# Kernel optimization log

Measured on AMD Instinct MI355X. Metric: run time of the kernel, lower is better.

The kernel has to match this reference:

```python
import jax, jax.numpy as jnp
import numpy as np

B, N, C, KV = 4, 4096, 1024, 1024
H = 4            # hardcoded 4-way split in the source
Ch, Kh = C // H, KV // H
EPS = 1e-5       # InstanceNorm2d default eps


def setup_inputs() -> dict:
    key = jax.random.key(0)
    ks = jax.random.split(key, 12)
    s = 0.02
    return {
        "emb1":     jax.random.normal(ks[0], (B, N, C),  jnp.float32),
        "emb_all":  jax.random.normal(ks[1], (B, N, KV), jnp.float32),
        "embd1":    jax.random.normal(ks[2], (B, N, C),  jnp.float32),
        "emb_alld": jax.random.normal(ks[3], (B, N, KV), jnp.float32),
        # per-head query weights (distinct per split), torch Linear layout [out,in]
        "Wq":   jax.random.normal(ks[4],  (H, Ch, Ch), jnp.float32) * s,
        "Wqd":  jax.random.normal(ks[5],  (H, Ch, Ch), jnp.float32) * s,
        # source reuses key[0]/value[0] for all splits -> single shared weight
        "Wk0":  jax.random.normal(ks[6],  (Kh, Kh), jnp.float32) * s,
        "Wv0":  jax.random.normal(ks[7],  (Kh, Kh), jnp.float32) * s,
        "Wkd0": jax.random.normal(ks[8],  (Kh, Kh), jnp.float32) * s,
        "Wvd0": jax.random.normal(ks[9],  (Kh, Kh), jnp.float32) * s,
        "Wout":  jax.random.normal(ks[10], (C, C), jnp.float32) * s,
        "Woutd": jax.random.normal(ks[11], (C, C), jnp.float32) * s,
    }


def _inorm(s):
    # InstanceNorm2d(affine=False): normalize over the (C/4, KV/4) plane per (b, head)
    m = s.mean(axis=(2, 3), keepdims=True)
    v = ((s - m) ** 2).mean(axis=(2, 3), keepdims=True)
    return (s - m) * jax.lax.rsqrt(v + EPS)


def reference(emb1, emb_all, embd1, emb_alld,
              Wq, Wqd, Wk0, Wv0, Wkd0, Wvd0, Wout, Woutd):
    scale = 1.0 / np.sqrt(KV).astype(np.float32)
    # split into 4 channel groups and project (Q: per-group weight; K/V: shared weight)
    Q  = jnp.einsum('bnhc,hoc->bhno', emb1.reshape(B, N, H, Ch),  Wq)    # [B,H,N,Ch]
    Qd = jnp.einsum('bnhc,hoc->bhno', embd1.reshape(B, N, H, Ch), Wqd)
    K  = jnp.einsum('bnhk,ok->bhno', emb_all.reshape(B, N, H, Kh),  Wk0)  # [B,H,N,Kh]
    V  = jnp.einsum('bnhk,ok->bhno', emb_all.reshape(B, N, H, Kh),  Wv0)
    Kd = jnp.einsum('bnhk,ok->bhno', emb_alld.reshape(B, N, H, Kh), Wkd0)
    Vd = jnp.einsum('bnhk,ok->bhno', emb_alld.reshape(B, N, H, Kh), Wvd0)
    # channel-attention scores: contract over tokens N -> [B,H,Ch,Kh]
    s1  = jnp.einsum('bhnc,bhnk->bhck', Q,  Kd) * scale
    sd1 = jnp.einsum('bhnc,bhnk->bhck', Qd, K)  * scale
    p1  = jax.nn.softmax(_inorm(s1),  axis=-1)
    pd1 = jax.nn.softmax(_inorm(sd1), axis=-1)
    # context: probs @ V^T -> [b,h,c,n]; permute(0,3,2,1)+view -> [B,N,C] (c-major, h-minor)
    ctx1  = jnp.einsum('bhck,bhnk->bnch', p1,  Vd).reshape(B, N, C)
    ctxd1 = jnp.einsum('bhck,bhnk->bnch', pd1, V ).reshape(B, N, C)
    O1  = ctx1  @ Wout.T
    Od1 = ctxd1 @ Woutd.T
    return (O1, Od1)
```

## Files before the change

### kernel.cpp

```cpp
#include <hip/hip_runtime.h>
#include <math.h>


#define PITCH 40

typedef __bf16 bf16x4 __attribute__((ext_vector_type(4)));
typedef __bf16 bf16x8 __attribute__((ext_vector_type(8)));
typedef float f32x4 __attribute__((ext_vector_type(4)));

__device__ inline void gl2lds16(const void* g, void* l) {
    __builtin_amdgcn_global_load_lds(
        (const __attribute__((address_space(1))) unsigned int*)g,
        (__attribute__((address_space(3))) unsigned int*)l, 16, 0, 0);
}

__global__ __launch_bounds__(256) void prep_x(const float* __restrict__ emb_all,
                                              const float* __restrict__ emb_alld,
                                              __bf16* __restrict__ Xb) {
    const float* src = blockIdx.y ? emb_alld : emb_all;
    __bf16* dst = Xb + (long long)blockIdx.y * 16777216;
    long long i4 = (long long)blockIdx.x * 256 + threadIdx.x;
    float4 v = *(const float4*)&src[i4 * 4];
    bf16x4 o = {(__bf16)v.x, (__bf16)v.y, (__bf16)v.z, (__bf16)v.w};
    *(bf16x4*)&dst[i4 * 4] = o;
}

__global__ __launch_bounds__(256) void prep_w(
    const float* __restrict__ Wq, const float* __restrict__ Wqd,
    const float* __restrict__ Wk0, const float* __restrict__ Wv0,
    const float* __restrict__ Wkd0, const float* __restrict__ Wvd0,
    const float* __restrict__ Wout, const float* __restrict__ Woutd,
    __bf16* __restrict__ Wq_bf, __bf16* __restrict__ Wk_bf,
    __bf16* __restrict__ WvT_bf, __bf16* __restrict__ WoutR_bf)
{
    int id = blockIdx.x * 256 + threadIdx.x;
    if (id < 524288) {
        Wq_bf[id] = (__bf16)(id < 262144 ? Wq[id] : Wqd[id - 262144]);
    } else if (id < 655360) {
        int j = id - 524288;
        Wk_bf[j] = (__bf16)(j < 65536 ? Wkd0[j] : Wk0[j - 65536]);
    } else if (id < 786432) {
        int j = id - 655360;
        int p = j >> 16, r = (j >> 8) & 255, c2 = j & 255;
        const float* s = p ? Wv0 : Wvd0;
        WvT_bf[j] = (__bf16)s[c2 * 256 + r];
    } else if (id < 2883584) {
        int j = id - 786432;
        int p = j >> 20; int rem = j & 1048575; int h = rem >> 18; int oc = rem & 262143;
        int o = oc >> 8, c = oc & 255;
        const float* s = p ? Woutd : Wout;
        WoutR_bf[j] = (__bf16)s[o * 1024 + c * 4 + h];
    }
}

__global__ __launch_bounds__(256) void gram_mfma(
    const float* __restrict__ emb1, const float* __restrict__ emb_all,
    const float* __restrict__ embd1, const float* __restrict__ emb_alld,
    float* __restrict__ Gpart)
{
    __shared__ __bf16 As[128 * PITCH];
    __shared__ __bf16 Bs[128 * PITCH];

    const int z = blockIdx.z;
    const int path = z >> 4, bh = z & 15;
    const int b = bh >> 2, h = bh & 3;
    const float* Xm = (path == 0 ? emb_alld : emb_all) + (long long)b * 4194304 + h * 256;
    const float* Xn = (path == 0 ? emb1     : embd1)   + (long long)b * 4194304 + h * 256;

    const int i0 = (blockIdx.x >> 1) * 128;
    const int j0 = (blockIdx.x & 1) * 128;
    const int kb0 = blockIdx.y * 1024;

    const int t = threadIdx.x;
    const int q  = t & 7;
    const int i4 = t >> 3;
    const int lane = t & 63;
    const int wave = t >> 6;
    const int wr = (wave >> 1) * 64, wc = (wave & 1) * 64;
    const int fm = lane & 15, fg = lane >> 4;

    f32x4 acc[4][4];
#pragma unroll
    for (int u = 0; u < 4; ++u)
#pragma unroll
        for (int v = 0; v < 4; ++v) acc[u][v] = (f32x4){0.f, 0.f, 0.f, 0.f};

    for (int kb = kb0; kb < kb0 + 1024; kb += 32) {
        float4 va[4], vb[4];
        const float* pa = Xm + (long long)(kb + q * 4) * 1024 + i0 + i4 * 4;
        const float* pb = Xn + (long long)(kb + q * 4) * 1024 + j0 + i4 * 4;
#pragma unroll
        for (int r = 0; r < 4; ++r) {
            va[r] = *(const float4*)(pa + (long long)r * 1024);
            vb[r] = *(const float4*)(pb + (long long)r * 1024);
        }
        __syncthreads();
#pragma unroll
        for (int c = 0; c < 4; ++c) {
            bf16x4 wa, wb;
#pragma unroll
            for (int r = 0; r < 4; ++r) {
                wa[r] = (__bf16)(((const float*)&va[r])[c]);
                wb[r] = (__bf16)(((const float*)&vb[r])[c]);
            }
            *(bf16x4*)&As[(i4 * 4 + c) * PITCH + q * 4] = wa;
            *(bf16x4*)&Bs[(i4 * 4 + c) * PITCH + q * 4] = wb;
        }
        __syncthreads();

        bf16x8 af[4], bfv[4];
#pragma unroll
        for (int mt = 0; mt < 4; ++mt)
            af[mt] = *(const bf16x8*)&As[(wr + mt * 16 + fm) * PITCH + fg * 8];
#pragma unroll
        for (int nt = 0; nt < 4; ++nt)
            bfv[nt] = *(const bf16x8*)&Bs[(wc + nt * 16 + fm) * PITCH + fg * 8];
#pragma unroll
        for (int mt = 0; mt < 4; ++mt)
#pragma unroll
            for (int nt = 0; nt < 4; ++nt)
                acc[mt][nt] = __builtin_amdgcn_mfma_f32_16x16x32_bf16(af[mt], bfv[nt], acc[mt][nt], 0, 0, 0);
    }

    float* Gp = Gpart + ((long long)blockIdx.y * 32 + z) * 65536;
    const int col = lane & 15, rq = (lane >> 4) * 4;
#pragma unroll
    for (int mt = 0; mt < 4; ++mt)
#pragma unroll
        for (int nt = 0; nt < 4; ++nt)
#pragma unroll
            for (int r = 0; r < 4; ++r)
                Gp[(i0 + wr + mt * 16 + rq + r) * 256 + (j0 + wc + nt * 16 + col)] = acc[mt][nt][r];
}

__global__ __launch_bounds__(256) void reduce_g(const float* __restrict__ Gpart, __bf16* __restrict__ GT) {
    long long idx4 = (long long)blockIdx.x * 256 + threadIdx.x;
    float4 a = *(const float4*)&Gpart[idx4 * 4];
    float4 b = *(const float4*)&Gpart[2097152 + idx4 * 4];
    float4 c = *(const float4*)&Gpart[4194304 + idx4 * 4];
    float4 d = *(const float4*)&Gpart[6291456 + idx4 * 4];
    bf16x4 o;
    o[0] = (__bf16)(a.x + b.x + c.x + d.x);
    o[1] = (__bf16)(a.y + b.y + c.y + d.y);
    o[2] = (__bf16)(a.z + b.z + c.z + d.z);
    o[3] = (__bf16)(a.w + b.w + c.w + d.w);
    *(bf16x4*)&GT[idx4 * 4] = o;
}

template <typename CT>
__global__ __launch_bounds__(256) void mfma_nt(
    const __bf16* __restrict__ A, const __bf16* __restrict__ B, CT* __restrict__ C,
    int mtiles, int K,
    long long a1, long long a2, long long a3,
    long long b1, long long b2, long long b3,
    long long c1, long long c2, long long c3,
    int cpitch, float alpha)
{
    __shared__ __bf16 As[64 * 32];
    __shared__ __bf16 Bs[64 * 32];
    const int z = blockIdx.y;
    const __bf16* Az = A + (long long)(z >> 4) * a1 + (long long)((z >> 2) & 3) * a2 + (long long)(z & 3) * a3;
    const __bf16* Bz = B + (long long)(z >> 4) * b1 + (long long)((z >> 2) & 3) * b2 + (long long)(z & 3) * b3;
    CT* Cz = C + (long long)(z >> 4) * c1 + (long long)((z >> 2) & 3) * c2 + (long long)(z & 3) * c3;

    const int tm = blockIdx.x % mtiles, tn = blockIdx.x / mtiles;
    const int t = threadIdx.x;
    const int lane = t & 63, wave = t >> 6;
    const int row = t >> 2, ch = t & 3;
    const int fm = lane & 15, fg = lane >> 4;

    const __bf16* ga = Az + (long long)(tm * 64 + row) * K + ch * 8;
    const __bf16* gb = Bz + (long long)(tn * 64 + row) * K + ch * 8;
    __bf16* la = &As[t * 8];
    __bf16* lb = &Bs[t * 8];

    f32x4 acc[4];
#pragma unroll
    for (int u = 0; u < 4; ++u) acc[u] = (f32x4){0.f, 0.f, 0.f, 0.f};

    for (int kb = 0; kb < K; kb += 32) {
        __syncthreads();
        gl2lds16(ga + kb, la);
        gl2lds16(gb + kb, lb);
        __syncthreads();
        bf16x8 bv = *(const bf16x8*)&Bs[(wave * 16 + fm) * 32 + fg * 8];
#pragma unroll
        for (int mt = 0; mt < 4; ++mt) {
            bf16x8 av = *(const bf16x8*)&As[(mt * 16 + fm) * 32 + fg * 8];
            acc[mt] = __builtin_amdgcn_mfma_f32_16x16x32_bf16(av, bv, acc[mt], 0, 0, 0);
        }
    }

    const int colc = tn * 64 + wave * 16 + fm;
    const int rq = fg * 4;
#pragma unroll
    for (int mt = 0; mt < 4; ++mt)
#pragma unroll
        for (int r = 0; r < 4; ++r) {
            int rowc = tm * 64 + mt * 16 + rq + r;
            Cz[(long long)rowc * cpitch + colc] = (CT)(acc[mt][r] * alpha);
        }
}


#define VMCNT8 asm volatile("s_waitcnt vmcnt(8)" ::: "memory")
#define VMCNT0 asm volatile("s_waitcnt vmcnt(0)" ::: "memory")
#define BARR   asm volatile("s_barrier" ::: "memory")

#define STAGE_A(h, kt, c) do { \
    _Pragma("unroll") \
    for (int o = 0; o < 2; ++o) { \
        int rl = (h) * 64 + o * 128 + stg_row; \
        gl2lds16(Xa + (long long)rl * 1024 + (kt) * 64 + stg_col, \
                 &lds[(c) * 32768 + rl * 64 + lin_col]); \
    } \
} while (0)

#define STAGE_B(h, kt, c) do { \
    _Pragma("unroll") \
    for (int o = 0; o < 2; ++o) { \
        int rl = o * 128 + (h) * 32 + (stg_row & 31) + ((stg_row & 32) << 1); \
        gl2lds16(Bb + (long long)rl * 1024 + (kt) * 64 + stg_col, \
                 &lds[(c) * 32768 + 16384 + rl * 64 + lin_col]); \
    } \
} while (0)

#define LOAD_A(hm, c) do { \
    _Pragma("unroll") \
    for (int mt = 0; mt < 4; ++mt) { \
        const __bf16* p = &lds[(c) * 32768 + (wr * 128 + (hm) * 64 + mt * 16 + fm) * 64]; \
        af[mt][0] = *(const bf16x8*)&p[(fg * 8) ^ rsw]; \
        af[mt][1] = *(const bf16x8*)&p[(32 + fg * 8) ^ rsw]; \
    } \
} while (0)

#define LOAD_B(hn, c) do { \
    _Pragma("unroll") \
    for (int nt = 0; nt < 2; ++nt) { \
        const __bf16* p = &lds[(c) * 32768 + 16384 + (wc * 64 + (hn) * 32 + nt * 16 + fm) * 64]; \
        bv[(hn) * 2 + nt][0] = *(const bf16x8*)&p[(fg * 8) ^ rsw]; \
        bv[(hn) * 2 + nt][1] = *(const bf16x8*)&p[(32 + fg * 8) ^ rsw]; \
    } \
} while (0)

#define MFMA_Q(hm, hn) do { \
    __builtin_amdgcn_s_setprio(1); \
    _Pragma("unroll") \
    for (int mt = 0; mt < 4; ++mt) \
        _Pragma("unroll") \
        for (int nt = 0; nt < 2; ++nt) { \
            acc[(hm) * 4 + mt][(hn) * 2 + nt] = __builtin_amdgcn_mfma_f32_16x16x32_bf16( \
                af[mt][0], bv[(hn) * 2 + nt][0], acc[(hm) * 4 + mt][(hn) * 2 + nt], 0, 0, 0); \
            acc[(hm) * 4 + mt][(hn) * 2 + nt] = __builtin_amdgcn_mfma_f32_16x16x32_bf16( \
                af[mt][1], bv[(hn) * 2 + nt][1], acc[(hm) * 4 + mt][(hn) * 2 + nt], 0, 0, 0); \
        } \
    __builtin_amdgcn_s_setprio(0); \
} while (0)

__global__ __launch_bounds__(512, 2) void obig8(
    const __bf16* __restrict__ Xall, const __bf16* __restrict__ Mb, float* __restrict__ out)
{
    __shared__ __bf16 lds[65536];

    const int id = blockIdx.x;
    const int wg = (id & 7) * 64 + (id >> 3);
    const int z = wg >> 6;
    const int tile = wg & 63;
    const int tm = tile & 15, tn = tile >> 4;
    const int path = z >> 2, b = z & 3;

    const __bf16* Xa = Xall + (path == 0 ? 16777216LL : 0LL)
                     + (long long)b * 4194304 + (long long)tm * 262144;
    const __bf16* Bb = Mb + (long long)path * 4194304 + (long long)b * 1048576
                     + (long long)tn * 262144;
    float* Ob = out + (long long)path * 16777216 + (long long)b * 4194304;

    const int t = threadIdx.x;
    const int lane = t & 63, wave = t >> 6;
    const int wr = wave >> 2, wc = wave & 3;
    const int fm = lane & 15, fg = lane >> 4;
    const int stg_row = t >> 3;
    const int lin_col = (t & 7) * 8;
    const int stg_col = ((t & 7) ^ (stg_row & 7)) * 8;
    const int rsw = (fm & 7) * 8;

    f32x4 acc[8][4];
#pragma unroll
    for (int u = 0; u < 8; ++u)
#pragma unroll
        for (int v = 0; v < 4; ++v) acc[u][v] = (f32x4){0.f, 0.f, 0.f, 0.f};

    bf16x8 af[4][2];
    bf16x8 bv[8][2];

    STAGE_A(0, 0, 0); STAGE_B(0, 0, 0); STAGE_B(1, 0, 0); STAGE_A(1, 0, 0);
    STAGE_A(0, 1, 1); STAGE_B(0, 1, 1); STAGE_B(1, 1, 1); STAGE_A(1, 1, 1);
    VMCNT8;
    BARR;

    for (int kt = 0; kt < 14; ++kt) {
        const int c = kt & 1;
        LOAD_A(0, c);
        LOAD_B(0, c);
        BARR;
        MFMA_Q(0, 0);
        BARR;
        LOAD_B(1, c);
        STAGE_A(0, kt + 2, c);
        BARR;
        MFMA_Q(0, 1);
        BARR;
        LOAD_A(1, c);
        STAGE_B(0, kt + 2, c);
        BARR;
        MFMA_Q(1, 1);
        BARR;
        STAGE_B(1, kt + 2, c);
        STAGE_A(1, kt + 2, c);
        VMCNT8;
        BARR;
        MFMA_Q(1, 0);
        BARR;
    }

    {
        LOAD_A(0, 0);
        LOAD_B(0, 0);
        BARR;
        MFMA_Q(0, 0);
        BARR;
        LOAD_B(1, 0);
        BARR;
        MFMA_Q(0, 1);
        BARR;
        LOAD_A(1, 0);
        BARR;
        MFMA_Q(1, 1);
        BARR;
        VMCNT0;
        BARR;
        MFMA_Q(1, 0);
        BARR;
    }

    {
        LOAD_A(0, 1);
        LOAD_B(0, 1);
        MFMA_Q(0, 0);
        LOAD_B(1, 1);
        MFMA_Q(0, 1);
        LOAD_A(1, 1);
        MFMA_Q(1, 1);
        MFMA_Q(1, 0);
    }

    const int rq = fg * 4;
    float* op = Ob + (long long)(tm * 256 + wr * 128 + rq) * 1024 + tn * 256 + wc * 64 + fm;
#pragma unroll
    for (int mi = 0; mi < 8; ++mi)
#pragma unroll
        for (int ni = 0; ni < 4; ++ni)
#pragma unroll
            for (int r = 0; r < 4; ++r)
                op[(long long)(mi * 16 + r) * 1024 + ni * 16] = acc[mi][ni][r];
}

__global__ __launch_bounds__(256) void stats_kernel(const float* __restrict__ S, float* __restrict__ st) {
    int pg = blockIdx.x;
    const float* s = S + (long long)pg * 65536;
    float sum = 0.f, sq = 0.f;
    for (int i = threadIdx.x; i < 65536; i += 256) {
        float v = s[i];
        sum += v;
        sq += v * v;
    }
#pragma unroll
    for (int off = 32; off; off >>= 1) {
        sum += __shfl_down(sum, off);
        sq  += __shfl_down(sq,  off);
    }
    __shared__ float r1[4], r2[4];
    int w = threadIdx.x >> 6;
    if ((threadIdx.x & 63) == 0) { r1[w] = sum; r2[w] = sq; }
    __syncthreads();
    if (threadIdx.x == 0) {
        float ts = r1[0] + r1[1] + r1[2] + r1[3];
        float tq = r2[0] + r2[1] + r2[2] + r2[3];
        float mean = ts * (1.0f / 65536.0f);
        float var = tq * (1.0f / 65536.0f) - mean * mean;
        st[pg * 2 + 0] = mean;
        st[pg * 2 + 1] = rsqrtf(var + 1e-5f);
    }
}

__global__ __launch_bounds__(256) void softmax_kernel(const float* __restrict__ S,
                                                      const float* __restrict__ st,
                                                      __bf16* __restrict__ p_bf) {
    int pg = blockIdx.y;
    int c = blockIdx.x;
    float mean = st[pg * 2 + 0], rstd = st[pg * 2 + 1];
    const float* row = S + (long long)pg * 65536 + c * 256;
    int t = threadIdx.x;
    float x = (row[t] - mean) * rstd;
    float m = x;
#pragma unroll
    for (int off = 32; off; off >>= 1) m = fmaxf(m, __shfl_down(m, off));
    __shared__ float r1[4], r2[4];
    int w = t >> 6;
    if ((t & 63) == 0) r1[w] = m;
    __syncthreads();
    m = fmaxf(fmaxf(r1[0], r1[1]), fmaxf(r1[2], r1[3]));
    float e = expf(x - m);
    float ssum = e;
#pragma unroll
    for (int off = 32; off; off >>= 1) ssum += __shfl_down(ssum, off);
    if ((t & 63) == 0) r2[w] = ssum;
    __syncthreads();
    ssum = r2[0] + r2[1] + r2[2] + r2[3];
    p_bf[(long long)pg * 65536 + c * 256 + t] = (__bf16)(e / ssum);
}

extern "C" void kernel_launch(void* const* d_in, const int* in_sizes, int n_in,
                              void* d_out, int out_size, void* d_ws, size_t ws_size,
                              hipStream_t stream) {
    const float* emb1     = (const float*)d_in[0];
    const float* emb_all  = (const float*)d_in[1];
    const float* embd1    = (const float*)d_in[2];
    const float* emb_alld = (const float*)d_in[3];
    const float* Wq    = (const float*)d_in[4];
    const float* Wqd   = (const float*)d_in[5];
    const float* Wk0   = (const float*)d_in[6];
    const float* Wv0   = (const float*)d_in[7];
    const float* Wkd0  = (const float*)d_in[8];
    const float* Wvd0  = (const float*)d_in[9];
    const float* Wout  = (const float*)d_in[10];
    const float* Woutd = (const float*)d_in[11];
    float* out = (float*)d_out;

    float* ws = (float*)d_ws;
    float*  Gpart   = ws;
    __bf16* Mb_bf   = (__bf16*)ws;
    __bf16* X_bf    = (__bf16*)(ws + 8388608);
    __bf16* GT_bf   = (__bf16*)(ws + 25165824);
    __bf16* T_bf    = (__bf16*)(ws + 26214400);
    float*  S       = ws + 27262976;
    __bf16* p_bf    = (__bf16*)(ws + 29360128);
    __bf16* PT_bf   = (__bf16*)(ws + 30408704);
    __bf16* Wq_bf   = (__bf16*)(ws + 31457280);
    __bf16* Wk_bf   = (__bf16*)(ws + 31719424);
    __bf16* WvT_bf  = (__bf16*)(ws + 31784960);
    __bf16* WoutR_bf= (__bf16*)(ws + 31850496);
    float*  st      = ws + 32899072;

    dim3 blk(256);

    prep_x<<<dim3(16384, 2), blk, 0, stream>>>(emb_all, emb_alld, X_bf);
    prep_w<<<11264, blk, 0, stream>>>(Wq, Wqd, Wk0, Wv0, Wkd0, Wvd0, Wout, Woutd,
                                      Wq_bf, Wk_bf, WvT_bf, WoutR_bf);

    gram_mfma<<<dim3(4, 4, 32), blk, 0, stream>>>(emb1, emb_all, embd1, emb_alld, Gpart);
    reduce_g<<<2048, blk, 0, stream>>>(Gpart, GT_bf);

    mfma_nt<__bf16><<<dim3(16, 32), blk, 0, stream>>>(
        Wq_bf, GT_bf, T_bf, 4, 256,
        262144, 0, 65536,  1048576, 262144, 65536,  1048576, 262144, 65536, 256, 1.0f);
    mfma_nt<float><<<dim3(16, 32), blk, 0, stream>>>(
        T_bf, Wk_bf, S, 4, 256,
        1048576, 262144, 65536,  65536, 0, 0,  1048576, 262144, 65536, 256, 0.03125f);

    stats_kernel<<<32, blk, 0, stream>>>(S, st);
    softmax_kernel<<<dim3(256, 32), blk, 0, stream>>>(S, st, p_bf);

    mfma_nt<__bf16><<<dim3(16, 32), blk, 0, stream>>>(
        WvT_bf, p_bf, PT_bf, 4, 256,
        65536, 0, 0,  1048576, 262144, 65536,  1048576, 262144, 65536, 256, 1.0f);
    mfma_nt<__bf16><<<dim3(64, 32), blk, 0, stream>>>(
        WoutR_bf, PT_bf, Mb_bf, 16, 256,
        1048576, 0, 262144,  1048576, 262144, 65536,  4194304, 1048576, 256, 1024, 1.0f);

    obig8<<<dim3(512), dim3(512), 0, stream>>>(X_bf, Mb_bf, out);
}
```

Measured before the change: 567.9 us.

## Double-buffer gram kernel loads and parallelize instance-norm stats and softmax

The gram kernel now keeps two register sets and two LDS buffers, so global loads for the next k-slice are issued while the current slice is converted and fed to MFMA, and one of the two barriers per step is dropped. The stats kernel is split across 8 chunks per plane with float4 loads, and the softmax kernel folds those partials together. Softmax now handles one row per wave with shuffle-xor reductions instead of a block-wide reduction over shared memory. This trades more registers and LDS in the gram kernel (it also declares a min-blocks hint of 2) for less load latency exposure and less serial work in the small kernels.

Result: faster. 507.5 us (-10.6%).

```diff
diff --git a/kernel.cpp b/kernel.cpp
--- a/kernel.cpp
+++ b/kernel.cpp
@@ -53,13 +53,13 @@
     }
 }
 
-__global__ __launch_bounds__(256) void gram_mfma(
+__global__ __launch_bounds__(256, 2) void gram_mfma(
     const float* __restrict__ emb1, const float* __restrict__ emb_all,
     const float* __restrict__ embd1, const float* __restrict__ emb_alld,
     float* __restrict__ Gpart)
 {
-    __shared__ __bf16 As[128 * PITCH];
-    __shared__ __bf16 Bs[128 * PITCH];
+    __shared__ __bf16 As[2][128 * PITCH];
+    __shared__ __bf16 Bs[2][128 * PITCH];
 
     const int z = blockIdx.z;
     const int path = z >> 4, bh = z & 15;
@@ -85,42 +85,59 @@
 #pragma unroll
         for (int v = 0; v < 4; ++v) acc[u][v] = (f32x4){0.f, 0.f, 0.f, 0.f};
 
-    for (int kb = kb0; kb < kb0 + 1024; kb += 32) {
-        float4 va[4], vb[4];
-        const float* pa = Xm + (long long)(kb + q * 4) * 1024 + i0 + i4 * 4;
-        const float* pb = Xn + (long long)(kb + q * 4) * 1024 + j0 + i4 * 4;
-#pragma unroll
-        for (int r = 0; r < 4; ++r) {
-            va[r] = *(const float4*)(pa + (long long)r * 1024);
-            vb[r] = *(const float4*)(pb + (long long)r * 1024);
-        }
-        __syncthreads();
-#pragma unroll
-        for (int c = 0; c < 4; ++c) {
-            bf16x4 wa, wb;
-#pragma unroll
-            for (int r = 0; r < 4; ++r) {
-                wa[r] = (__bf16)(((const float*)&va[r])[c]);
-                wb[r] = (__bf16)(((const float*)&vb[r])[c]);
-            }
-            *(bf16x4*)&As[(i4 * 4 + c) * PITCH + q * 4] = wa;
-            *(bf16x4*)&Bs[(i4 * 4 + c) * PITCH + q * 4] = wb;
-        }
-        __syncthreads();
-
-        bf16x8 af[4], bfv[4];
-#pragma unroll
-        for (int mt = 0; mt < 4; ++mt)
-            af[mt] = *(const bf16x8*)&As[(wr + mt * 16 + fm) * PITCH + fg * 8];
-#pragma unroll
-        for (int nt = 0; nt < 4; ++nt)
-            bfv[nt] = *(const bf16x8*)&Bs[(wc + nt * 16 + fm) * PITCH + fg * 8];
-#pragma unroll
-        for (int mt = 0; mt < 4; ++mt)
-#pragma unroll
-            for (int nt = 0; nt < 4; ++nt)
-                acc[mt][nt] = __builtin_amdgcn_mfma_f32_16x16x32_bf16(af[mt], bfv[nt], acc[mt][nt], 0, 0, 0);
-    }
+    const float* pa = Xm + (long long)(kb0 + q * 4) * 1024 + i0 + i4 * 4;
+    const float* pb = Xn + (long long)(kb0 + q * 4) * 1024 + j0 + i4 * 4;
+
+    float4 vaA[4], vbA[4], vaB[4], vbB[4];
+#pragma unroll
+    for (int r = 0; r < 4; ++r) {
+        vaA[r] = *(const float4*)(pa + (long long)r * 1024);
+        vbA[r] = *(const float4*)(pb + (long long)r * 1024);
+    }
+
+#define GRAM_STEP(CURA, CURB, NXTA, NXTB, BUF, SOFF, GUARD)                         \
+    do {                                                                            \
+        if (GUARD) {                                                                \
+            const float* qa = pa + (long long)(SOFF) * 32768;                       \
+            const float* qb = pb + (long long)(SOFF) * 32768;                       \
+            _Pragma("unroll")                                                       \
+            for (int r = 0; r < 4; ++r) {                                           \
+                NXTA[r] = *(const float4*)(qa + (long long)r * 1024);               \
+                NXTB[r] = *(const float4*)(qb + (long long)r * 1024);               \
+            }                                                                       \
+        }                                                                           \
+        _Pragma("unroll")                                                           \
+        for (int cc = 0; cc < 4; ++cc) {                                            \
+            bf16x4 wa, wb;                                                          \
+            _Pragma("unroll")                                                       \
+            for (int r = 0; r < 4; ++r) {                                           \
+                wa[r] = (__bf16)(((const float*)&CURA[r])[cc]);                     \
+                wb[r] = (__bf16)(((const float*)&CURB[r])[cc]);                     \
+            }                                                                       \
+            *(bf16x4*)&As[BUF][(i4 * 4 + cc) * PITCH + q * 4] = wa;                 \
+            *(bf16x4*)&Bs[BUF][(i4 * 4 + cc) * PITCH + q * 4] = wb;                 \
+        }                                                                           \
+        asm volatile("s_waitcnt lgkmcnt(0)\ns_barrier" ::: "memory");               \
+        bf16x8 af[4], bfv[4];                                                       \
+        _Pragma("unroll")                                                           \
+        for (int mt = 0; mt < 4; ++mt)                                              \
+            af[mt] = *(const bf16x8*)&As[BUF][(wr + mt * 16 + fm) * PITCH + fg * 8];\
+        _Pragma("unroll")                                                           \
+        for (int nt = 0; nt < 4; ++nt)                                              \
+            bfv[nt] = *(const bf16x8*)&Bs[BUF][(wc + nt * 16 + fm) * PITCH + fg * 8];\
+        _Pragma("unroll")                                                           \
+        for (int mt = 0; mt < 4; ++mt)                                              \
+            _Pragma("unroll")                                                       \
+            for (int nt = 0; nt < 4; ++nt)                                          \
+                acc[mt][nt] = __builtin_amdgcn_mfma_f32_16x16x32_bf16(              \
+                    af[mt], bfv[nt], acc[mt][nt], 0, 0, 0);                         \
+    } while (0)
+
+    for (int s = 0; s < 32; s += 2) {
+        GRAM_STEP(vaA, vbA, vaB, vbB, 0, s + 1, true);
+        GRAM_STEP(vaB, vbB, vaA, vbA, 1, s + 2, (s < 30));
+    }
+#undef GRAM_STEP
 
     float* Gp = Gpart + ((long long)blockIdx.y * 32 + z) * 65536;
     const int col = lane & 15, rq = (lane >> 4) * 4;
@@ -365,14 +382,17 @@
                 op[(long long)(mi * 16 + r) * 1024 + ni * 16] = acc[mi][ni][r];
 }
 
-__global__ __launch_bounds__(256) void stats_kernel(const float* __restrict__ S, float* __restrict__ st) {
-    int pg = blockIdx.x;
-    const float* s = S + (long long)pg * 65536;
+__global__ __launch_bounds__(256) void stats1_kernel(const float* __restrict__ S,
+                                                     float* __restrict__ pstat) {
+    const int ch = blockIdx.x, pg = blockIdx.y;
+    const float* s = S + (long long)pg * 65536 + ch * 8192;
+    const int t = threadIdx.x;
     float sum = 0.f, sq = 0.f;
-    for (int i = threadIdx.x; i < 65536; i += 256) {
-        float v = s[i];
-        sum += v;
-        sq += v * v;
+#pragma unroll
+    for (int i = 0; i < 8; ++i) {
+        float4 v = *(const float4*)&s[(i * 256 + t) * 4];
+        sum += v.x + v.y + v.z + v.w;
+        sq += v.x * v.x + v.y * v.y + v.z * v.z + v.w * v.w;
     }
 #pragma unroll
     for (int off = 32; off; off >>= 1) {
@@ -380,44 +400,44 @@
         sq  += __shfl_down(sq,  off);
     }
     __shared__ float r1[4], r2[4];
-    int w = threadIdx.x >> 6;
-    if ((threadIdx.x & 63) == 0) { r1[w] = sum; r2[w] = sq; }
+    int w = t >> 6;
+    if ((t & 63) == 0) { r1[w] = sum; r2[w] = sq; }
     __syncthreads();
-    if (threadIdx.x == 0) {
-        float ts = r1[0] + r1[1] + r1[2] + r1[3];
-        float tq = r2[0] + r2[1] + r2[2] + r2[3];
-        float mean = ts * (1.0f / 65536.0f);
-        float var = tq * (1.0f / 65536.0f) - mean * mean;
-        st[pg * 2 + 0] = mean;
-        st[pg * 2 + 1] = rsqrtf(var + 1e-5f);
+    if (t == 0) {
+        pstat[(pg * 8 + ch) * 2 + 0] = r1[0] + r1[1] + r1[2] + r1[3];
+        pstat[(pg * 8 + ch) * 2 + 1] = r2[0] + r2[1] + r2[2] + r2[3];
     }
 }
 
 __global__ __launch_bounds__(256) void softmax_kernel(const float* __restrict__ S,
-                                                      const float* __restrict__ st,
+                                                      const float* __restrict__ pstat,
                                                       __bf16* __restrict__ p_bf) {
-    int pg = blockIdx.y;
-    int c = blockIdx.x;
-    float mean = st[pg * 2 + 0], rstd = st[pg * 2 + 1];
+    const int pg = blockIdx.y;
+    float ts = 0.f, tq = 0.f;
+#pragma unroll
+    for (int i = 0; i < 8; ++i) {
+        ts += pstat[(pg * 8 + i) * 2 + 0];
+        tq += pstat[(pg * 8 + i) * 2 + 1];
+    }
+    const float mean = ts * (1.0f / 65536.0f);
+    const float rstd = rsqrtf(tq * (1.0f / 65536.0f) - mean * mean + 1e-5f);
+
+    const int wave = threadIdx.x >> 6, lane = threadIdx.x & 63;
+    const int c = blockIdx.x * 4 + wave;
     const float* row = S + (long long)pg * 65536 + c * 256;
-    int t = threadIdx.x;
-    float x = (row[t] - mean) * rstd;
-    float m = x;
-#pragma unroll
-    for (int off = 32; off; off >>= 1) m = fmaxf(m, __shfl_down(m, off));
-    __shared__ float r1[4], r2[4];
-    int w = t >> 6;
-    if ((t & 63) == 0) r1[w] = m;
-    __syncthreads();
-    m = fmaxf(fmaxf(r1[0], r1[1]), fmaxf(r1[2], r1[3]));
-    float e = expf(x - m);
-    float ssum = e;
-#pragma unroll
-    for (int off = 32; off; off >>= 1) ssum += __shfl_down(ssum, off);
-    if ((t & 63) == 0) r2[w] = ssum;
-    __syncthreads();
-    ssum = r2[0] + r2[1] + r2[2] + r2[3];
-    p_bf[(long long)pg * 65536 + c * 256 + t] = (__bf16)(e / ssum);
+    float4 v = *(const float4*)&row[lane * 4];
+    float x0 = (v.x - mean) * rstd, x1 = (v.y - mean) * rstd;
+    float x2 = (v.z - mean) * rstd, x3 = (v.w - mean) * rstd;
+    float m = fmaxf(fmaxf(x0, x1), fmaxf(x2, x3));
+#pragma unroll
+    for (int off = 32; off; off >>= 1) m = fmaxf(m, __shfl_xor(m, off));
+    float e0 = expf(x0 - m), e1 = expf(x1 - m), e2 = expf(x2 - m), e3 = expf(x3 - m);
+    float ssum = e0 + e1 + e2 + e3;
+#pragma unroll
+    for (int off = 32; off; off >>= 1) ssum += __shfl_xor(ssum, off);
+    float inv = 1.0f / ssum;
+    bf16x4 o = {(__bf16)(e0 * inv), (__bf16)(e1 * inv), (__bf16)(e2 * inv), (__bf16)(e3 * inv)};
+    *(bf16x4*)&p_bf[(long long)pg * 65536 + c * 256 + lane * 4] = o;
 }
 
 extern "C" void kernel_launch(void* const* d_in, const int* in_sizes, int n_in,
@@ -468,8 +488,8 @@
         T_bf, Wk_bf, S, 4, 256,
         1048576, 262144, 65536,  65536, 0, 0,  1048576, 262144, 65536, 256, 0.03125f);
 
-    stats_kernel<<<32, blk, 0, stream>>>(S, st);
-    softmax_kernel<<<dim3(256, 32), blk, 0, stream>>>(S, st, p_bf);
+    stats1_kernel<<<dim3(8, 32), blk, 0, stream>>>(S, st);
+    softmax_kernel<<<dim3(64, 32), blk, 0, stream>>>(S, st, p_bf);
 
     mfma_nt<__bf16><<<dim3(16, 32), blk, 0, stream>>>(
         WvT_bf, p_bf, PT_bf, 4, 256,
```
